# Performance work log

Hardware: AMD Instinct MI355X
Metric: run time of the kernel (lower is better)

The kernel has to match this reference:

```python
import jax, jax.numpy as jnp
import numpy as np

N = 20000      # num nodes
E = 320000     # num edges (avg degree 16)
F_IN = 518     # object_feature_dim
D = 128        # node_embedding_dim (= GAT out_channels)
ED = 32        # edge_embedding_dim
R = 26         # num_relations
H = 4          # GAT heads (concat=False -> mean over heads)
HID = 256      # node_encoder hidden


def _gat_layer(x, src, dst, ea, lin, lin_e, att_s, att_d, att_e, bias):
    """PyG GATConv: add_self_loops=True (fill_value='mean'), concat=False, negative_slope=0.2."""
    n = x.shape[0]
    ones = jnp.ones((src.shape[0],), x.dtype)
    cnt = jax.ops.segment_sum(ones, dst, num_segments=n)                    # [N]
    loop_ea = jax.ops.segment_sum(ea, dst, num_segments=n) / jnp.maximum(cnt, 1.0)[:, None]
    idx = jnp.arange(n)
    s = jnp.concatenate([src, idx])
    d = jnp.concatenate([dst, idx])
    ea2 = jnp.concatenate([ea, loop_ea], axis=0)                            # [E+N, ED]
    h = (x @ lin).reshape(n, H, D)                                          # [N,H,D]
    a_s = jnp.einsum('nhd,hd->nh', h, att_s)                                # [N,H]
    a_d = jnp.einsum('nhd,hd->nh', h, att_d)
    e = (ea2 @ lin_e).reshape(-1, H, D)                                     # [E+N,H,D]
    a_e = jnp.einsum('ehd,hd->eh', e, att_e)
    alpha = jax.nn.leaky_relu(a_s[s] + a_d[d] + a_e, 0.2)                   # [E+N,H]
    amax = jax.ops.segment_max(alpha, d, num_segments=n)
    alpha = jnp.exp(alpha - amax[d])
    denom = jax.ops.segment_sum(alpha, d, num_segments=n)
    alpha = alpha / (denom[d] + 1e-16)                                      # segment softmax
    msg = h[s] * alpha[:, :, None]                                          # [E+N,H,D]
    out = jax.ops.segment_sum(msg, d, num_segments=n)                       # [N,H,D]
    return out.mean(axis=1) + bias                                          # concat=False


def setup_inputs() -> dict:
    key = jax.random.key(0)
    ks = jax.random.split(key, 18)
    g = lambda k, shp, s=0.05: jax.random.normal(k, shp, jnp.float32) * s
    return {
        'x': g(ks[0], (N, F_IN), 1.0),
        'edge_index': jax.random.randint(ks[1], (2, E), 0, N),
        'edge_type': jax.random.randint(ks[2], (E,), 0, R),
        'w1': g(ks[3], (F_IN, HID)), 'b1': jnp.zeros((HID,), jnp.float32),
        'w2': g(ks[4], (HID, D)),    'b2': jnp.zeros((D,), jnp.float32),
        'rel_emb': g(ks[5], (R, ED), 1.0),
        'lin1': g(ks[6], (D, H * D)), 'line1': g(ks[7], (ED, H * D)),
        'atts1': g(ks[8], (H, D)), 'attd1': g(ks[9], (H, D)), 'atte1': g(ks[10], (H, D)),
        'bias1': jnp.zeros((D,), jnp.float32),
        'lin2': g(ks[11], (D, H * D)), 'line2': g(ks[12], (ED, H * D)),
        'atts2': g(ks[13], (H, D)), 'attd2': g(ks[14], (H, D)), 'atte2': g(ks[15], (H, D)),
        'bias2': jnp.zeros((D,), jnp.float32),
    }


def reference(x, edge_index, edge_type, w1, b1, w2, b2, rel_emb,
              lin1, line1, atts1, attd1, atte1, bias1,
              lin2, line2, atts2, attd2, atte2, bias2):
    src, dst = edge_index[0], edge_index[1]
    # node encoder (dropout inactive in eval)
    h = jax.nn.relu(x @ w1 + b1) @ w2 + b2                                  # [N,D]
    ea = rel_emb[edge_type]                                                 # [E,ED]
    h = jax.nn.relu(_gat_layer(h, src, dst, ea, lin1, line1, atts1, attd1, atte1, bias1))
    h = jax.nn.relu(_gat_layer(h, src, dst, ea, lin2, line2, atts2, attd2, atte2, bias2))
    return h
```

## Files before the change

kernel.cpp:

```cpp
#include <hip/hip_runtime.h>
#include <math.h>

#define N_NODES 20000
#define MP      20032
#define N_EDGES 320000
#define F_IN    518
#define HIDDEN  256
#define DIM     128
#define NH      4

typedef __attribute__((ext_vector_type(8))) short bf16x8;
typedef __attribute__((ext_vector_type(4))) float f32x4;
typedef unsigned short ushort_t;

__device__ __forceinline__ float lrelu02(float x) { return x > 0.f ? x : 0.2f * x; }

__device__ __forceinline__ void gl_lds16(const void* g, void* l) {
    __builtin_amdgcn_global_load_lds(
        (const __attribute__((address_space(1))) unsigned int*)g,
        (__attribute__((address_space(3))) unsigned int*)l, 16, 0, 0);
}

__device__ __forceinline__ unsigned int hi16(float v) { return __float_as_uint(v) >> 16; }
__device__ __forceinline__ unsigned int lo16(float v) {
    unsigned int h = __float_as_uint(v) & 0xFFFF0000u;
    return __float_as_uint(v - __uint_as_float(h)) >> 16;
}
__device__ __forceinline__ unsigned int rnd16(float v) {
    unsigned int u = __float_as_uint(v);
    return (u + 0x7FFFu + ((u >> 16) & 1u)) >> 16;
}
__device__ __forceinline__ float bfl(unsigned int u) { return __uint_as_float(u << 16); }
__device__ __forceinline__ float bfh(unsigned int u) { return __uint_as_float(u & 0xFFFF0000u); }

__global__ __launch_bounds__(256, 4) void gemm_mfma_v2(
    const ushort_t* __restrict__ Ah, const ushort_t* __restrict__ Al,
    const ushort_t* __restrict__ Bh, const ushort_t* __restrict__ Bl,
    const float* __restrict__ bias,
    int M, int K8, int N, int act,
    float* __restrict__ Cf,
    ushort_t* __restrict__ Ch, ushort_t* __restrict__ Cl,
    ushort_t* __restrict__ Cb,
    ushort_t* __restrict__ Ca)
{
    __shared__ __align__(16) ushort_t lds[12288];
    const int tid = threadIdx.x;
    const int w = tid >> 6, lane = tid & 63;
    const int row0 = blockIdx.y * 64, col0 = blockIdx.x * 128;
    const int nkb = K8 >> 2;
    const int m16 = lane & 15, q = lane >> 4;
    const bool use_al = (Al != nullptr);

    f32x4 acc[4][2] = {};

    for (int kb = 0; kb < nkb; ++kb) {
        const size_t kc = (size_t)(kb * 4 + w);
        const size_t aoff = (kc * MP + row0) * 8 + lane * 8;
        const size_t boff = (kc * N + col0) * 8 + lane * 8;
        gl_lds16(Ah + aoff, &lds[w * 512]);
        if (use_al) gl_lds16(Al + aoff, &lds[2048 + w * 512]);
        gl_lds16(Bh + boff,       &lds[4096 + w * 1024]);
        gl_lds16(Bh + boff + 512, &lds[4096 + w * 1024 + 512]);
        gl_lds16(Bl + boff,       &lds[8192 + w * 1024]);
        gl_lds16(Bl + boff + 512, &lds[8192 + w * 1024 + 512]);
        __syncthreads();

        bf16x8 fah[4], fal[4], fbh[2], fbl[2];
        const int fa = q * 512 + m16 * 8;
        #pragma unroll
        for (int mi = 0; mi < 4; ++mi) {
            fah[mi] = *(const bf16x8*)&lds[fa + mi * 128];
            if (use_al) fal[mi] = *(const bf16x8*)&lds[2048 + fa + mi * 128];
        }
        const int fb = q * 1024 + (w * 32 + m16) * 8;
        #pragma unroll
        for (int ni = 0; ni < 2; ++ni) {
            fbh[ni] = *(const bf16x8*)&lds[4096 + fb + ni * 128];
            fbl[ni] = *(const bf16x8*)&lds[8192 + fb + ni * 128];
        }
        #pragma unroll
        for (int mi = 0; mi < 4; ++mi)
            #pragma unroll
            for (int ni = 0; ni < 2; ++ni) {
                acc[mi][ni] = __builtin_amdgcn_mfma_f32_16x16x32_bf16(fah[mi], fbh[ni], acc[mi][ni], 0, 0, 0);
                acc[mi][ni] = __builtin_amdgcn_mfma_f32_16x16x32_bf16(fah[mi], fbl[ni], acc[mi][ni], 0, 0, 0);
            }
        if (use_al) {
            #pragma unroll
            for (int mi = 0; mi < 4; ++mi)
                #pragma unroll
                for (int ni = 0; ni < 2; ++ni)
                    acc[mi][ni] = __builtin_amdgcn_mfma_f32_16x16x32_bf16(fal[mi], fbh[ni], acc[mi][ni], 0, 0, 0);
        }
        __syncthreads();
    }

    #pragma unroll
    for (int ni = 0; ni < 2; ++ni) {
        const int col = col0 + w * 32 + ni * 16 + m16;
        const float bb = bias ? bias[col] : 0.f;
        #pragma unroll
        for (int mi = 0; mi < 4; ++mi) {
            #pragma unroll
            for (int r = 0; r < 4; ++r) {
                const int row = row0 + mi * 16 + q * 4 + r;
                if (row < M) {
                    float v = acc[mi][ni][r] + bb;
                    if (act) v = fmaxf(v, 0.f);
                    if (Cf) Cf[(size_t)row * N + col] = v;
                    if (Cb) Cb[(size_t)row * N + col] = (ushort_t)rnd16(v);
                    const size_t p = (((size_t)(col >> 3)) * MP + row) * 8 + (col & 7);
                    if (Ch) { Ch[p] = (ushort_t)hi16(v); Cl[p] = (ushort_t)lo16(v); }
                    if (Ca) Ca[p] = (ushort_t)rnd16(v);
                }
            }
        }
    }
}

__global__ __launch_bounds__(256) void conv_a_t_kernel(
    const float* __restrict__ x, ushort_t* __restrict__ xh, ushort_t* __restrict__ xl)
{
    __shared__ float tile[64][68];
    const int tid = threadIdx.x;
    const int r0 = blockIdx.x * 64;
    const int c0 = blockIdx.y * 64;

    #pragma unroll
    for (int it = 0; it < 4; ++it) {
        const int r = (tid >> 4) + it * 16;
        const int c = (tid & 15) * 4;
        const int gr = r0 + r, gc = c0 + c;
        float4 v = {0.f, 0.f, 0.f, 0.f};
        if (gr < N_NODES) {
            if (gc + 3 < F_IN) {
                v = *(const float4*)(x + (size_t)gr * F_IN + gc);
            } else {
                float tmp[4] = {0.f, 0.f, 0.f, 0.f};
                #pragma unroll
                for (int u = 0; u < 4; ++u)
                    if (gc + u < F_IN) tmp[u] = x[(size_t)gr * F_IN + gc + u];
                v.x = tmp[0]; v.y = tmp[1]; v.z = tmp[2]; v.w = tmp[3];
            }
        }
        tile[r][c] = v.x; tile[r][c+1] = v.y; tile[r][c+2] = v.z; tile[r][c+3] = v.w;
    }
    __syncthreads();

    const int k8l = tid >> 5;
    const int k8 = (c0 >> 3) + k8l;
    if (k8 >= 68) return;
    const int rr = (tid & 31) * 2;
    #pragma unroll
    for (int u = 0; u < 2; ++u) {
        const int r = rr + u;
        unsigned int hp[4], lp[4];
        #pragma unroll
        for (int i = 0; i < 4; ++i) {
            const float v0 = tile[r][k8l * 8 + 2 * i];
            const float v1 = tile[r][k8l * 8 + 2 * i + 1];
            hp[i] = (hi16(v1) << 16) | hi16(v0);
            lp[i] = (lo16(v1) << 16) | lo16(v0);
        }
        const size_t p = ((size_t)k8 * MP + r0 + r) * 8;
        *(uint4*)(xh + p) = make_uint4(hp[0], hp[1], hp[2], hp[3]);
        *(uint4*)(xl + p) = make_uint4(lp[0], lp[1], lp[2], lp[3]);
    }
}

#define W1_T (68 * 256 * 8)
#define W2_T (32 * 128 * 8)
#define L_T  (16 * 512 * 8)
__global__ __launch_bounds__(256) void conv_w_all_kernel(
    const float* __restrict__ w1, const float* __restrict__ w2,
    const float* __restrict__ l0, const float* __restrict__ l1,
    ushort_t* __restrict__ w1h, ushort_t* __restrict__ w1l,
    ushort_t* __restrict__ w2h, ushort_t* __restrict__ w2l,
    ushort_t* __restrict__ l0h, ushort_t* __restrict__ l0l,
    ushort_t* __restrict__ l1h, ushort_t* __restrict__ l1l)
{
    int idx = blockIdx.x * 256 + threadIdx.x;
    const float* w; ushort_t *bh, *bl; int K, N, local;
    if (idx < W1_T) { w = w1; bh = w1h; bl = w1l; K = F_IN; N = HIDDEN; local = idx; }
    else if (idx < W1_T + W2_T) { w = w2; bh = w2h; bl = w2l; K = HIDDEN; N = DIM; local = idx - W1_T; }
    else if (idx < W1_T + W2_T + L_T) { w = l0; bh = l0h; bl = l0l; K = DIM; N = 512; local = idx - W1_T - W2_T; }
    else if (idx < W1_T + W2_T + 2 * L_T) { w = l1; bh = l1h; bl = l1l; K = DIM; N = 512; local = idx - W1_T - W2_T - L_T; }
    else return;
    const int j = local & 7;
    const int rem = local >> 3;
    const int n = rem % N;
    const int k = (rem / N) * 8 + j;
    const float v = (k < K) ? w[(size_t)k * N + n] : 0.f;
    bh[local] = (ushort_t)hi16(v);
    bl[local] = (ushort_t)lo16(v);
}

__global__ __launch_bounds__(256) void wa2_kernel(
    const float* __restrict__ lin0, const float* __restrict__ lin1,
    const float* __restrict__ atts0, const float* __restrict__ attd0,
    const float* __restrict__ atts1, const float* __restrict__ attd1,
    float* __restrict__ wa_s0, float* __restrict__ wa_d0,
    float* __restrict__ wa_s1, float* __restrict__ wa_d1)
{
    const int wrk = blockIdx.x * 256 + threadIdx.x;
    if (wrk >= 2048) return;
    const int L = wrk >> 10;
    const int sd = (wrk >> 9) & 1;
    const int p = wrk & 511;
    const int h = p >> 7, d = p & 127;
    const float* lin = L ? lin1 : lin0;
    const float* av = L ? (sd ? attd1 : atts1) : (sd ? attd0 : atts0);
    float* out = L ? (sd ? wa_d1 : wa_s1) : (sd ? wa_d0 : wa_s0);
    const float* lp = lin + (size_t)d * (NH * DIM) + h * DIM;
    const float* ap = av + h * DIM;
    float acc = 0.f;
    #pragma unroll 8
    for (int i = 0; i < DIM; ++i) acc += lp[i] * ap[i];
    out[h * DIM + d] = acc;
}

__global__ __launch_bounds__(256) void as_ad_kernel(
    const float* __restrict__ xb, const float* __restrict__ wa_s,
    const float* __restrict__ wa_d, float* __restrict__ a_s, float* __restrict__ a_d)
{
    const int gw = blockIdx.x * 4 + (threadIdx.x >> 6);
    const int lane = threadIdx.x & 63;
    if (gw >= N_NODES * NH) return;
    const int n = gw >> 2, h = gw & 3;
    const float* hp = xb + (size_t)n * DIM;
    float2 hv = *(const float2*)(hp + lane * 2);
    float2 sv = *(const float2*)(wa_s + h * DIM + lane * 2);
    float2 dv = *(const float2*)(wa_d + h * DIM + lane * 2);
    float s = hv.x * sv.x + hv.y * sv.y;
    float d = hv.x * dv.x + hv.y * dv.y;
    #pragma unroll
    for (int off = 32; off > 0; off >>= 1) {
        s += __shfl_down(s, off);
        d += __shfl_down(d, off);
    }
    if (lane == 0) { a_s[n * 4 + h] = s; a_d[n * 4 + h] = d; }
}

__global__ __launch_bounds__(128) void rel_table2_kernel(
    const float* __restrict__ rel_emb,
    const float* __restrict__ line0, const float* __restrict__ atte0,
    const float* __restrict__ line1, const float* __restrict__ atte1,
    float* __restrict__ table)
{
    __shared__ float we[32][NH];
    const int L = blockIdx.x;
    const float* line = L ? line1 : line0;
    const float* atte = L ? atte1 : atte0;
    float* tab = table + L * 128;
    const int tid = threadIdx.x;
    const int k = tid >> 2, h = tid & 3;
    float acc = 0.f;
    for (int d = 0; d < DIM; ++d)
        acc += line[(size_t)k * (NH * DIM) + h * DIM + d] * atte[h * DIM + d];
    we[k][h] = acc;
    __syncthreads();
    if (tid < 26 * NH) {
        int r = tid >> 2, hh = tid & 3;
        float t = 0.f;
        for (int kk = 0; kk < 32; ++kk) t += rel_emb[r * 32 + kk] * we[kk][hh];
        tab[r * 4 + hh] = t;
    }
}

__global__ __launch_bounds__(256) void hist_kernel(
    const int* __restrict__ dst, int* __restrict__ cnt)
{
    const int e = blockIdx.x * blockDim.x + threadIdx.x;
    if (e >= N_EDGES) return;
    atomicAdd(&cnt[dst[e]], 1);
}

__global__ __launch_bounds__(1024) void scan_kernel(
    const int* __restrict__ cnt, int* __restrict__ ptr, int* __restrict__ ptr_copy)
{
    __shared__ int tsum[1024];
    const int tid = threadIdx.x;
    const int CH = 20;
    const int base = tid * CH;
    int s = 0;
    #pragma unroll
    for (int i = 0; i < CH; ++i) {
        int idx = base + i;
        if (idx < N_NODES) s += cnt[idx];
    }
    tsum[tid] = s;
    __syncthreads();
    for (int off = 1; off < 1024; off <<= 1) {
        int v = (tid >= off) ? tsum[tid - off] : 0;
        __syncthreads();
        tsum[tid] += v;
        __syncthreads();
    }
    int run = (tid == 0) ? 0 : tsum[tid - 1];
    #pragma unroll
    for (int i = 0; i < CH; ++i) {
        int idx = base + i;
        if (idx < N_NODES) {
            ptr[idx] = run;
            ptr_copy[idx] = run;
            run += cnt[idx];
        }
    }
    if (tid == 0) ptr[N_NODES] = N_EDGES;
}

__global__ __launch_bounds__(256) void scatter_kernel(
    const int* __restrict__ src, const int* __restrict__ dst, const int* __restrict__ etype,
    int* __restrict__ ptr_copy, int2* __restrict__ se)
{
    const int e = blockIdx.x * blockDim.x + threadIdx.x;
    if (e >= N_EDGES) return;
    const int d = dst[e];
    const int pos = atomicAdd(&ptr_copy[d], 1);
    se[pos] = make_int2(src[e], etype[e]);
}

__global__ __launch_bounds__(256) void node_agg2_kernel(
    const int* __restrict__ ptr, const int2* __restrict__ se,
    const float* __restrict__ a_s, const float* __restrict__ a_d,
    const float* __restrict__ table, const ushort_t* __restrict__ hb,
    const float* __restrict__ bias,
    float* __restrict__ outf, ushort_t* __restrict__ oa,
    const float* __restrict__ wa_s2, const float* __restrict__ wa_d2,
    float* __restrict__ a_s2, float* __restrict__ a_d2)
{
    __shared__ float red[2][64][11];
    const int tid = threadIdx.x;
    const int wave = tid >> 6, lane = tid & 63;
    const int slot = wave >> 1, half = wave & 1;
    const int n = blockIdx.x * 2 + slot;
    const int head = lane >> 4;
    const int cbase = lane * 8;
    const int beg = ptr[n], end = ptr[n + 1];
    const int mid = beg + ((end - beg + 1) >> 1);
    const int lo = half ? mid : beg;
    const int hi = half ? end : mid;
    const float adh = a_d[n * 4 + head];

    float acc[8] = {};
    float dh = 0.f, eh = 0.f;

    int j = lo;
    for (; j + 2 <= hi; j += 2) {
        const int2 E0 = se[j], E1 = se[j + 1];
        const uint4 g0 = *(const uint4*)(hb + (size_t)E0.x * 512 + cbase);
        const uint4 g1 = *(const uint4*)(hb + (size_t)E1.x * 512 + cbase);
        const float a0 = a_s[E0.x * 4 + head];
        const float t0 = table[E0.y * 4 + head];
        const float a1 = a_s[E1.x * 4 + head];
        const float t1 = table[E1.y * 4 + head];
        const float p0 = __expf(lrelu02(a0 + adh + t0));
        const float p1 = __expf(lrelu02(a1 + adh + t1));
        eh += t0 + t1;
        dh += p0 + p1;
        acc[0] += p0 * bfl(g0.x) + p1 * bfl(g1.x);
        acc[1] += p0 * bfh(g0.x) + p1 * bfh(g1.x);
        acc[2] += p0 * bfl(g0.y) + p1 * bfl(g1.y);
        acc[3] += p0 * bfh(g0.y) + p1 * bfh(g1.y);
        acc[4] += p0 * bfl(g0.z) + p1 * bfl(g1.z);
        acc[5] += p0 * bfh(g0.z) + p1 * bfh(g1.z);
        acc[6] += p0 * bfl(g0.w) + p1 * bfl(g1.w);
        acc[7] += p0 * bfh(g0.w) + p1 * bfh(g1.w);
    }
    if (j < hi) {
        const int2 E0 = se[j];
        const uint4 g0 = *(const uint4*)(hb + (size_t)E0.x * 512 + cbase);
        const float a0 = a_s[E0.x * 4 + head];
        const float t0 = table[E0.y * 4 + head];
        const float p0 = __expf(lrelu02(a0 + adh + t0));
        eh += t0; dh += p0;
        acc[0] += p0 * bfl(g0.x); acc[1] += p0 * bfh(g0.x);
        acc[2] += p0 * bfl(g0.y); acc[3] += p0 * bfh(g0.y);
        acc[4] += p0 * bfl(g0.z); acc[5] += p0 * bfh(g0.z);
        acc[6] += p0 * bfl(g0.w); acc[7] += p0 * bfh(g0.w);
    }

    if (half == 1) {
        #pragma unroll
        for (int k = 0; k < 8; ++k) red[slot][lane][k] = acc[k];
        red[slot][lane][8] = dh;
        red[slot][lane][9] = eh;
    }
    __syncthreads();
    if (half == 1) return;

    #pragma unroll
    for (int k = 0; k < 8; ++k) acc[k] += red[slot][lane][k];
    dh += red[slot][lane][8];
    eh += red[slot][lane][9];

    const float inv = 1.0f / fmaxf((float)(end - beg), 1.0f);
    const float ps = __expf(lrelu02(a_s[n * 4 + head] + adh + eh * inv));
    dh += ps;
    {
        const uint4 gs = *(const uint4*)(hb + (size_t)n * 512 + cbase);
        acc[0] += ps * bfl(gs.x); acc[1] += ps * bfh(gs.x);
        acc[2] += ps * bfl(gs.y); acc[3] += ps * bfh(gs.y);
        acc[4] += ps * bfl(gs.z); acc[5] += ps * bfh(gs.z);
        acc[6] += ps * bfl(gs.w); acc[7] += ps * bfh(gs.w);
    }

    const float ih = 0.25f / (dh + 1e-16f);
    float t[8];
    #pragma unroll
    for (int k = 0; k < 8; ++k) {
        t[k] = acc[k] * ih;
        t[k] += __shfl_xor(t[k], 16);
        t[k] += __shfl_xor(t[k], 32);
    }
    if (lane < 16) {
        const float4 b0 = *(const float4*)(bias + cbase);
        const float4 b1 = *(const float4*)(bias + cbase + 4);
        float o[8];
        o[0] = fmaxf(t[0] + b0.x, 0.f); o[1] = fmaxf(t[1] + b0.y, 0.f);
        o[2] = fmaxf(t[2] + b0.z, 0.f); o[3] = fmaxf(t[3] + b0.w, 0.f);
        o[4] = fmaxf(t[4] + b1.x, 0.f); o[5] = fmaxf(t[5] + b1.y, 0.f);
        o[6] = fmaxf(t[6] + b1.z, 0.f); o[7] = fmaxf(t[7] + b1.w, 0.f);
        if (outf) {
            float4 v0 = {o[0], o[1], o[2], o[3]};
            float4 v1 = {o[4], o[5], o[6], o[7]};
            *(float4*)(outf + (size_t)n * DIM + cbase) = v0;
            *(float4*)(outf + (size_t)n * DIM + cbase + 4) = v1;
        }
        if (oa) {
            unsigned int up[4];
            #pragma unroll
            for (int i = 0; i < 4; ++i)
                up[i] = (rnd16(o[2*i+1]) << 16) | rnd16(o[2*i]);
            *(uint4*)(oa + ((size_t)lane * MP + n) * 8) = make_uint4(up[0], up[1], up[2], up[3]);
        }
        if (wa_s2) {
            float pss[4] = {0,0,0,0}, pdd[4] = {0,0,0,0};
            #pragma unroll
            for (int h = 0; h < NH; ++h) {
                const float* ws = wa_s2 + h * DIM + cbase;
                const float* wd = wa_d2 + h * DIM + cbase;
                #pragma unroll
                for (int i = 0; i < 8; ++i) {
                    pss[h] += o[i] * ws[i];
                    pdd[h] += o[i] * wd[i];
                }
            }
            #pragma unroll
            for (int m = 1; m < 16; m <<= 1) {
                #pragma unroll
                for (int h = 0; h < NH; ++h) {
                    pss[h] += __shfl_xor(pss[h], m);
                    pdd[h] += __shfl_xor(pdd[h], m);
                }
            }
            if (lane == 0) {
                float4 vs = {pss[0], pss[1], pss[2], pss[3]};
                float4 vd = {pdd[0], pdd[1], pdd[2], pdd[3]};
                *(float4*)(a_s2 + n * 4) = vs;
                *(float4*)(a_d2 + n * 4) = vd;
            }
        }
    }
}

extern "C" void kernel_launch(void* const* d_in, const int* in_sizes, int n_in,
                              void* d_out, int out_size, void* d_ws, size_t ws_size,
                              hipStream_t stream)
{
    const float* x       = (const float*)d_in[0];
    const int*   eidx    = (const int*)d_in[1];
    const int*   etype   = (const int*)d_in[2];
    const float* w1      = (const float*)d_in[3];
    const float* b1      = (const float*)d_in[4];
    const float* w2      = (const float*)d_in[5];
    const float* b2      = (const float*)d_in[6];
    const float* rel_emb = (const float*)d_in[7];
    const float* lin[2]  = {(const float*)d_in[8],  (const float*)d_in[14]};
    const float* line[2] = {(const float*)d_in[9],  (const float*)d_in[15]};
    const float* atts[2] = {(const float*)d_in[10], (const float*)d_in[16]};
    const float* attd[2] = {(const float*)d_in[11], (const float*)d_in[17]};
    const float* atte[2] = {(const float*)d_in[12], (const float*)d_in[18]};
    const float* bias[2] = {(const float*)d_in[13], (const float*)d_in[19]};
    const int* src = eidx;
    const int* dst = eidx + N_EDGES;

    char* base = (char*)d_ws;
    size_t off = 0;
    auto alloc = [&](size_t bytes) -> void* {
        void* p = base + off;
        off = (off + bytes + 255) & ~(size_t)255;
        return p;
    };
    ushort_t* xh  = (ushort_t*)alloc((size_t)68 * MP * 8 * 2);
    ushort_t* xl  = (ushort_t*)alloc((size_t)68 * MP * 8 * 2);
    ushort_t* h1h = (ushort_t*)alloc((size_t)32 * MP * 8 * 2);
    ushort_t* h1l = (ushort_t*)alloc((size_t)32 * MP * 8 * 2);
    ushort_t* x0a = (ushort_t*)alloc((size_t)16 * MP * 8 * 2);
    void* reg1    = alloc((size_t)16 * MP * 8 * 4);
    ushort_t* w1h = (ushort_t*)alloc(W1_T * 2);
    ushort_t* w1l = (ushort_t*)alloc(W1_T * 2);
    ushort_t* w2h = (ushort_t*)alloc(W2_T * 2);
    ushort_t* w2l = (ushort_t*)alloc(W2_T * 2);
    ushort_t* l0h = (ushort_t*)alloc(L_T * 2);
    ushort_t* l0l = (ushort_t*)alloc(L_T * 2);
    ushort_t* l1h = (ushort_t*)alloc(L_T * 2);
    ushort_t* l1l = (ushort_t*)alloc(L_T * 2);
    float* a_s0  = (float*)alloc(N_NODES * 4 * 4);
    float* a_d0  = (float*)alloc(N_NODES * 4 * 4);
    float* a_s1  = (float*)alloc(N_NODES * 4 * 4);
    float* a_d1  = (float*)alloc(N_NODES * 4 * 4);
    float* table = (float*)alloc(2 * 128 * 4);
    float* wa_s0 = (float*)alloc(512 * 4);
    float* wa_d0 = (float*)alloc(512 * 4);
    float* wa_s1 = (float*)alloc(512 * 4);
    float* wa_d1 = (float*)alloc(512 * 4);
    int*  cnt_i  = (int*)alloc(N_NODES * 4);
    int*  ptr    = (int*)alloc((N_NODES + 4) * 4);
    int*  ptrc   = (int*)alloc(N_NODES * 4);
    int2* se     = (int2*)alloc((size_t)N_EDGES * 8);

    ushort_t* hb = xh;
    float* xbuf0 = (float*)reg1;
    ushort_t* x1a = (ushort_t*)reg1;

    const int mtiles = MP / 64;

    conv_a_t_kernel<<<dim3(MP / 64, 9), 256, 0, stream>>>(x, xh, xl);
    conv_w_all_kernel<<<(W1_T + W2_T + 2 * L_T + 255) / 256, 256, 0, stream>>>(
        w1, w2, lin[0], lin[1], w1h, w1l, w2h, w2l, l0h, l0l, l1h, l1l);
    wa2_kernel<<<8, 256, 0, stream>>>(lin[0], lin[1], atts[0], attd[0], atts[1], attd[1],
                                      wa_s0, wa_d0, wa_s1, wa_d1);
    rel_table2_kernel<<<2, 128, 0, stream>>>(rel_emb, line[0], atte[0], line[1], atte[1], table);

    hipMemsetAsync(cnt_i, 0, N_NODES * sizeof(int), stream);
    hist_kernel<<<(N_EDGES + 255) / 256, 256, 0, stream>>>(dst, cnt_i);
    scan_kernel<<<1, 1024, 0, stream>>>(cnt_i, ptr, ptrc);
    scatter_kernel<<<(N_EDGES + 255) / 256, 256, 0, stream>>>(src, dst, etype, ptrc, se);

    gemm_mfma_v2<<<dim3(HIDDEN / 128, mtiles), 256, 0, stream>>>(
        xh, xl, w1h, w1l, b1, N_NODES, 68, HIDDEN, 1, nullptr, h1h, h1l, nullptr, nullptr);
    gemm_mfma_v2<<<dim3(DIM / 128, mtiles), 256, 0, stream>>>(
        h1h, h1l, w2h, w2l, b2, N_NODES, 32, DIM, 0, xbuf0, nullptr, nullptr, nullptr, x0a);

    gemm_mfma_v2<<<dim3((NH * DIM) / 128, mtiles), 256, 0, stream>>>(
        x0a, nullptr, l0h, l0l, nullptr, N_NODES, 16, NH * DIM, 0, nullptr, nullptr, nullptr, hb, nullptr);
    as_ad_kernel<<<N_NODES, 256, 0, stream>>>(xbuf0, wa_s0, wa_d0, a_s0, a_d0);
    node_agg2_kernel<<<N_NODES / 2, 256, 0, stream>>>(
        ptr, se, a_s0, a_d0, table, hb, bias[0], nullptr, x1a,
        wa_s1, wa_d1, a_s1, a_d1);

    gemm_mfma_v2<<<dim3((NH * DIM) / 128, mtiles), 256, 0, stream>>>(
        x1a, nullptr, l1h, l1l, nullptr, N_NODES, 16, NH * DIM, 0, nullptr, nullptr, nullptr, hb, nullptr);
    node_agg2_kernel<<<N_NODES / 2, 256, 0, stream>>>(
        ptr, se, a_s1, a_d1, table + 128, hb, bias[1], (float*)d_out, nullptr,
        nullptr, nullptr, nullptr, nullptr);
}
```

Measured before the change: 426.0 us.

## Use one wave per node with software-pipelined edge gathers in aggregation

The aggregation kernel now gives each node a single wavefront instead of splitting its edge list across two waves and merging them through shared memory with a block barrier. It also software-pipelines the gather loop, issuing loads for the next pair of edges before computing the current pair, so memory latency overlaps with arithmetic. This removes the LDS reduction and __syncthreads, but each wave now walks twice as many edges serially and carries extra live registers for the prefetched data. The remainder loop becomes a general for loop.

```diff
diff --git a/kernel.cpp b/kernel.cpp
--- a/kernel.cpp
+++ b/kernel.cpp
@@ -320,7 +320,7 @@
     se[pos] = make_int2(src[e], etype[e]);
 }
 
-__global__ __launch_bounds__(256) void node_agg2_kernel(
+__global__ __launch_bounds__(256) void node_agg_p_kernel(
     const int* __restrict__ ptr, const int2* __restrict__ se,
     const float* __restrict__ a_s, const float* __restrict__ a_d,
     const float* __restrict__ table, const ushort_t* __restrict__ hb,
@@ -329,31 +329,40 @@
     const float* __restrict__ wa_s2, const float* __restrict__ wa_d2,
     float* __restrict__ a_s2, float* __restrict__ a_d2)
 {
-    __shared__ float red[2][64][11];
-    const int tid = threadIdx.x;
-    const int wave = tid >> 6, lane = tid & 63;
-    const int slot = wave >> 1, half = wave & 1;
-    const int n = blockIdx.x * 2 + slot;
+    const int n = blockIdx.x * 4 + (threadIdx.x >> 6);
+    const int lane = threadIdx.x & 63;
+    if (n >= N_NODES) return;
+    const int beg = ptr[n], end = ptr[n + 1];
     const int head = lane >> 4;
     const int cbase = lane * 8;
-    const int beg = ptr[n], end = ptr[n + 1];
-    const int mid = beg + ((end - beg + 1) >> 1);
-    const int lo = half ? mid : beg;
-    const int hi = half ? end : mid;
     const float adh = a_d[n * 4 + head];
 
     float acc[8] = {};
     float dh = 0.f, eh = 0.f;
 
-    int j = lo;
-    for (; j + 2 <= hi; j += 2) {
-        const int2 E0 = se[j], E1 = se[j + 1];
-        const uint4 g0 = *(const uint4*)(hb + (size_t)E0.x * 512 + cbase);
-        const uint4 g1 = *(const uint4*)(hb + (size_t)E1.x * 512 + cbase);
-        const float a0 = a_s[E0.x * 4 + head];
-        const float t0 = table[E0.y * 4 + head];
-        const float a1 = a_s[E1.x * 4 + head];
-        const float t1 = table[E1.y * 4 + head];
+    int j = beg;
+    uint4 ga, gb;
+    float aa, ta, ab, tb;
+    bool have = (j + 2 <= end);
+    if (have) {
+        const int2 Ea = se[j], Eb = se[j + 1];
+        ga = *(const uint4*)(hb + (size_t)Ea.x * 512 + cbase);
+        gb = *(const uint4*)(hb + (size_t)Eb.x * 512 + cbase);
+        aa = a_s[Ea.x * 4 + head]; ta = table[Ea.y * 4 + head];
+        ab = a_s[Eb.x * 4 + head]; tb = table[Eb.y * 4 + head];
+    }
+    while (have) {
+        const uint4 g0 = ga, g1 = gb;
+        const float a0 = aa, t0 = ta, a1 = ab, t1 = tb;
+        j += 2;
+        have = (j + 2 <= end);
+        if (have) {
+            const int2 Ea = se[j], Eb = se[j + 1];
+            ga = *(const uint4*)(hb + (size_t)Ea.x * 512 + cbase);
+            gb = *(const uint4*)(hb + (size_t)Eb.x * 512 + cbase);
+            aa = a_s[Ea.x * 4 + head]; ta = table[Ea.y * 4 + head];
+            ab = a_s[Eb.x * 4 + head]; tb = table[Eb.y * 4 + head];
+        }
         const float p0 = __expf(lrelu02(a0 + adh + t0));
         const float p1 = __expf(lrelu02(a1 + adh + t1));
         eh += t0 + t1;
@@ -367,7 +376,7 @@
         acc[6] += p0 * bfl(g0.w) + p1 * bfl(g1.w);
         acc[7] += p0 * bfh(g0.w) + p1 * bfh(g1.w);
     }
-    if (j < hi) {
+    for (; j < end; ++j) {
         const int2 E0 = se[j];
         const uint4 g0 = *(const uint4*)(hb + (size_t)E0.x * 512 + cbase);
         const float a0 = a_s[E0.x * 4 + head];
@@ -379,20 +388,6 @@
         acc[4] += p0 * bfl(g0.z); acc[5] += p0 * bfh(g0.z);
         acc[6] += p0 * bfl(g0.w); acc[7] += p0 * bfh(g0.w);
     }
-
-    if (half == 1) {
-        #pragma unroll
-        for (int k = 0; k < 8; ++k) red[slot][lane][k] = acc[k];
-        red[slot][lane][8] = dh;
-        red[slot][lane][9] = eh;
-    }
-    __syncthreads();
-    if (half == 1) return;
-
-    #pragma unroll
-    for (int k = 0; k < 8; ++k) acc[k] += red[slot][lane][k];
-    dh += red[slot][lane][8];
-    eh += red[slot][lane][9];
 
     const float inv = 1.0f / fmaxf((float)(end - beg), 1.0f);
     const float ps = __expf(lrelu02(a_s[n * 4 + head] + adh + eh * inv));
@@ -546,13 +541,13 @@
     gemm_mfma_v2<<<dim3((NH * DIM) / 128, mtiles), 256, 0, stream>>>(
         x0a, nullptr, l0h, l0l, nullptr, N_NODES, 16, NH * DIM, 0, nullptr, nullptr, nullptr, hb, nullptr);
     as_ad_kernel<<<N_NODES, 256, 0, stream>>>(xbuf0, wa_s0, wa_d0, a_s0, a_d0);
-    node_agg2_kernel<<<N_NODES / 2, 256, 0, stream>>>(
+    node_agg_p_kernel<<<(N_NODES + 3) / 4, 256, 0, stream>>>(
         ptr, se, a_s0, a_d0, table, hb, bias[0], nullptr, x1a,
         wa_s1, wa_d1, a_s1, a_d1);
 
     gemm_mfma_v2<<<dim3((NH * DIM) / 128, mtiles), 256, 0, stream>>>(
         x1a, nullptr, l1h, l1l, nullptr, N_NODES, 16, NH * DIM, 0, nullptr, nullptr, nullptr, hb, nullptr);
-    node_agg2_kernel<<<N_NODES / 2, 256, 0, stream>>>(
+    node_agg_p_kernel<<<(N_NODES + 3) / 4, 256, 0, stream>>>(
         ptr, se, a_s1, a_d1, table + 128, hb, bias[1], (float*)d_out, nullptr,
         nullptr, nullptr, nullptr, nullptr);
 }
```

After: 425.6 us. About the same (-0.1%).
